# Kernel tuning notes

Hardware: AMD Instinct MI355X
Metric: run time of the kernel (lower is better)

Reference implementation:

```python
import jax, jax.numpy as jnp
import numpy as np

H, IN, D, RD, A = 1024, 14, 100000, 10, 2

def setup_inputs() -> dict:
    key = jax.random.key(0)
    ks = jax.random.split(key, 12)
    f = lambda k, shp, s=1.0: jax.random.normal(k, shp, dtype=jnp.float32) * s
    return {
        "x_t": f(ks[0], (1, IN)),
        "h": f(ks[1], (1, 1, H), 0.1),
        "c": f(ks[2], (1, 1, H), 0.1),
        "keys": f(ks[3], (D, RD)),
        "vals": f(ks[4], (D, H)),
        "W_i2h": f(ks[5], (5 * H, IN), 0.1),
        "b_i2h": jnp.zeros((5 * H,), jnp.float32),
        "W_h2h": f(ks[6], (5 * H, H), 0.03),
        "b_h2h": jnp.zeros((5 * H,), jnp.float32),
        "W_ih": f(ks[7], (H, H), 0.03),
        "b_ih": jnp.zeros((H,), jnp.float32),
        "W_actor": f(ks[8], (A, H), 0.03),
        "b_actor": jnp.zeros((A,), jnp.float32),
        "W_critic": f(ks[9], (1, H), 0.03),
        "b_critic": jnp.zeros((1,), jnp.float32),
        "pick_arm": 0,
    }


def reference(x_t, h, c, keys, vals, W_i2h, b_i2h, W_h2h, b_h2h,
              W_ih, b_ih, W_actor, b_actor, W_critic, b_critic, pick_arm):
    Hd = W_h2h.shape[1]
    Rd = keys.shape[1]
    h2 = h.reshape(h.shape[1], -1)   # [1, H]
    c2 = c.reshape(c.shape[1], -1)   # [1, H]
    # fused i2h + h2h preactivation: [1, 5H]
    preact = x_t @ W_i2h.T + b_i2h + h2 @ W_h2h.T + b_h2h
    gates = jax.nn.sigmoid(preact[:, :4 * Hd])
    f_t = gates[:, :Hd]
    i_t = gates[:, Hd:2 * Hd]
    o_t = gates[:, 2 * Hd:3 * Hd]
    r_t = gates[:, 3 * Hd:4 * Hd]
    c_new = jnp.tanh(preact[:, 4 * Hd:])
    c_t = f_t * c2 + i_t * c_new
    # DND read: cosine similarity over stored keys, softmax-weighted value sum
    q = jax.lax.dynamic_slice(x_t[0], (pick_arm * Rd,), (Rd,))  # retrieval key
    dots = keys @ q                                              # [D]
    denom = jnp.maximum(jnp.linalg.norm(keys, axis=1) * jnp.linalg.norm(q), 1e-8)
    w = jax.nn.softmax(dots / denom)                             # [D]
    m_t = jnp.tanh(w @ vals)                                     # [H]
    c_t = c_t + r_t * m_t
    h_t = o_t * jnp.tanh(c_t)
    # A2C head (standard dnd-lstm A2C): shared relu layer, actor softmax, critic scalar
    hh = jax.nn.relu(h_t @ W_ih.T + b_ih)
    pi = jax.nn.softmax(hh @ W_actor.T + b_actor, axis=-1)       # [1, A]
    v = hh @ W_critic.T + b_critic                               # [1, 1]
    # categorical sampling with a fixed key (replaces torch.distributions sample)
    a = jax.random.categorical(jax.random.key(1), jnp.log(pi[0]))
    logp = jnp.log(pi[0, a])
    # pack: [pi(A), v(1), log_prob(1), h_t(H), c_t(H)]
    return jnp.concatenate([pi[0], v[0], logp[None], h_t[0], c_t[0]])
```

## Files before the change

kernel.cpp:

```cpp
#include <hip/hip_runtime.h>
#include <math.h>

#define NHID 1024
#define NIN 14
#define NKEYS 100000
#define NRD 10
#define R3 100
#define NB3 1000
#define NBPRE 1280
#define NSLOT 16
#define NPF 10

typedef float f32x4 __attribute__((ext_vector_type(4)));
typedef float f32x2 __attribute__((ext_vector_type(2)));

#define WS_MACC    0
#define WS_L       16384
#define WS_PREACT  16400
#define WS_HH      21520
#define ZERO_BYTES ((16384 + NSLOT) * 4)

__device__ inline float wave_reduce_sum(float v) {
#pragma unroll
    for (int off = 32; off > 0; off >>= 1) v += __shfl_down(v, off, 64);
    return v;
}

__device__ inline float sigm(float x) { return 1.0f / (1.0f + expf(-x)); }

__device__ inline float bcast_lane(float v, int lane) {
    return __uint_as_float(__builtin_amdgcn_readlane(__float_as_uint(v), lane));
}

__device__ inline void atomAddF(float* p, float v) { unsafeAtomicAdd(p, v); }

__device__ inline float load_q(const float* __restrict__ x, int pick, float* q) {
    int start = pick * NRD;
    if (start > NIN - NRD) start = NIN - NRD;
    if (start < 0) start = 0;
    float qn = 0.f;
#pragma unroll
    for (int k = 0; k < NRD; ++k) { q[k] = x[start + k]; qn = fmaf(q[k], q[k], qn); }
    return sqrtf(qn);
}

__device__ inline float score2(const float* __restrict__ keys, int i,
                               const float* q, float qn) {
    const f32x2* kp = (const f32x2*)(keys + (size_t)i * NRD);
    float dot = 0.f, kn = 0.f;
#pragma unroll
    for (int k = 0; k < 5; ++k) {
        f32x2 kv = kp[k];
        dot = fmaf(kv.x, q[2 * k], fmaf(kv.y, q[2 * k + 1], dot));
        kn  = fmaf(kv.x, kv.x, fmaf(kv.y, kv.y, kn));
    }
    return dot / fmaxf(sqrtf(kn) * qn, 1e-8f);
}

__global__ void __launch_bounds__(256) kA(const float* __restrict__ keys,
                                          const float* __restrict__ x,
                                          const int* __restrict__ pick_arm,
                                          const float* __restrict__ vals,
                                          float* __restrict__ macc,
                                          float* __restrict__ Lacc,
                                          const float* __restrict__ h,
                                          const float* __restrict__ Wi,
                                          const float* __restrict__ bi,
                                          const float* __restrict__ Wh,
                                          const float* __restrict__ bh,
                                          float* __restrict__ preact) {
    int tid = threadIdx.x;
    if (blockIdx.x < NB3) {
        int r0 = blockIdx.x * R3;
        int slot = blockIdx.x & (NSLOT - 1);
        int lane = tid & 63;
        const f32x4* vp = (const f32x4*)vals + ((size_t)r0 << 8) + tid;
        f32x4 buf[NPF];
#pragma unroll
        for (int j = 0; j < NPF; ++j)
            buf[j] = __builtin_nontemporal_load(&vp[(size_t)j << 8]);
        float q[NRD];
        float qn = load_q(x, pick_arm[0], q);
        float wva = expf(score2(keys, r0 + lane, q, qn));
        float wvb = 0.f;
        if (lane < R3 - 64)
            wvb = expf(score2(keys, r0 + 64 + lane, q, qn));
        if (tid < 64) {
            float ls = wave_reduce_sum(wva + wvb);
            if (tid == 0) atomAddF(&Lacc[slot], ls);
        }
        float ax = 0.f, ay = 0.f, az = 0.f, aw = 0.f;
#pragma unroll
        for (int r = 0; r < R3; ++r) {
            float w = (r < 64) ? bcast_lane(wva, r) : bcast_lane(wvb, r - 64);
            f32x4 v = buf[r % NPF];
            if (r + NPF < R3)
                buf[r % NPF] = __builtin_nontemporal_load(&vp[(size_t)(r + NPF) << 8]);
            ax = fmaf(w, v.x, ax);
            ay = fmaf(w, v.y, ay);
            az = fmaf(w, v.z, az);
            aw = fmaf(w, v.w, aw);
        }
        float* ms = macc + (size_t)slot * NHID;
        atomAddF(&ms[4 * tid + 0], ax);
        atomAddF(&ms[4 * tid + 1], ay);
        atomAddF(&ms[4 * tid + 2], az);
        atomAddF(&ms[4 * tid + 3], aw);
    } else {
        int wave = tid >> 6, lane = tid & 63;
        int row = (blockIdx.x - NB3) * 4 + wave;
        const f32x4* w4 = (const f32x4*)(Wh + (size_t)row * NHID);
        const f32x4* h4 = (const f32x4*)h;
        float p = 0.f;
#pragma unroll
        for (int j = 0; j < 4; ++j) {
            f32x4 wv = __builtin_nontemporal_load(&w4[j * 64 + lane]);
            f32x4 hv = h4[j * 64 + lane];
            p += wv.x * hv.x + wv.y * hv.y + wv.z * hv.z + wv.w * hv.w;
        }
        if (lane < NIN) p += x[lane] * Wi[(size_t)row * NIN + lane];
        p = wave_reduce_sum(p);
        if (lane == 0) preact[row] = p + bi[row] + bh[row];
    }
}

__global__ void __launch_bounds__(256) k45(const float* __restrict__ preact,
                                           const float* __restrict__ macc,
                                           const float* __restrict__ Lacc,
                                           const float* __restrict__ c_in,
                                           const float* __restrict__ Wih,
                                           const float* __restrict__ bih,
                                           float* __restrict__ out,
                                           float* __restrict__ hh) {
    __shared__ float hlds[NHID];
    int tid = threadIdx.x;
    float Ls = 0.f;
#pragma unroll
    for (int s = 0; s < NSLOT; ++s) Ls += Lacc[s];
    float invL = 1.0f / Ls;
    const f32x4* pre4 = (const f32x4*)preact;
    f32x4 fg = pre4[tid];
    f32x4 ig = pre4[256 + tid];
    f32x4 og = pre4[512 + tid];
    f32x4 rg = pre4[768 + tid];
    f32x4 gg = pre4[1024 + tid];
    f32x4 m4 = {0.f, 0.f, 0.f, 0.f};
#pragma unroll
    for (int s = 0; s < NSLOT; ++s) m4 += ((const f32x4*)(macc + (size_t)s * NHID))[tid];
    f32x4 c4 = ((const f32x4*)c_in)[tid];
    f32x4 h4, ct4;
#pragma unroll
    for (int e = 0; e < 4; ++e) {
        float f = sigm(fg[e]);
        float i = sigm(ig[e]);
        float o = sigm(og[e]);
        float r = sigm(rg[e]);
        float cn = tanhf(gg[e]);
        float mt = tanhf(m4[e] * invL);
        float ct = f * c4[e] + i * cn + r * mt;
        ct4[e] = ct;
        h4[e] = o * tanhf(ct);
    }
    ((f32x4*)hlds)[tid] = h4;
    if (blockIdx.x == 0) {
        ((f32x4*)(out + 4))[tid] = h4;
        ((f32x4*)(out + 4 + NHID))[tid] = ct4;
    }
    __syncthreads();
    int wave = tid >> 6, lane = tid & 63;
    int row = blockIdx.x * 4 + wave;
    const f32x4* w4 = (const f32x4*)(Wih + (size_t)row * NHID);
    const f32x4* hl4 = (const f32x4*)hlds;
    float p = 0.f;
#pragma unroll
    for (int j = 0; j < 4; ++j) {
        f32x4 wv = __builtin_nontemporal_load(&w4[j * 64 + lane]);
        f32x4 hv = hl4[j * 64 + lane];
        p += wv.x * hv.x + wv.y * hv.y + wv.z * hv.z + wv.w * hv.w;
    }
    p = wave_reduce_sum(p);
    if (lane == 0) hh[row] = fmaxf(p + bih[row], 0.f);
}

#define TF_ROUND(r) { x0 += x1; x1 = (x1 << r) | (x1 >> (32 - r)); x1 ^= x0; }

__global__ void k6_heads(const float* __restrict__ hh, const float* __restrict__ Wa,
                         const float* __restrict__ ba, const float* __restrict__ Wc,
                         const float* __restrict__ bc, float* __restrict__ out) {
    __shared__ float zz[3];
    int wave = threadIdx.x >> 6, lane = threadIdx.x & 63;
    if (wave < 3) {
        const float* W = (wave == 2) ? Wc : Wa + wave * NHID;
        const f32x4* w4 = (const f32x4*)W;
        const f32x4* h4 = (const f32x4*)hh;
        float p = 0.f;
#pragma unroll
        for (int j = 0; j < 4; ++j) {
            f32x4 wv = w4[j * 64 + lane];
            f32x4 hv = h4[j * 64 + lane];
            p += wv.x * hv.x + wv.y * hv.y + wv.z * hv.z + wv.w * hv.w;
        }
        p = wave_reduce_sum(p);
        if (lane == 0) zz[wave] = p;
    }
    __syncthreads();
    if (threadIdx.x == 0) {
        float z0 = zz[0] + ba[0], z1 = zz[1] + ba[1], v = zz[2] + bc[0];
        float mz = fmaxf(z0, z1);
        float e0 = expf(z0 - mz), e1 = expf(z1 - mz);
        float sum = e0 + e1;
        float pi0 = e0 / sum, pi1 = e1 / sum;
        float lse = mz + logf(sum);
        unsigned ks0 = 0u, ks1 = 1u, ks2 = 0u ^ 1u ^ 0x1BD11BDAu;
        unsigned x0 = 0u + ks0, x1 = 1u + ks1;
        TF_ROUND(13) TF_ROUND(15) TF_ROUND(26) TF_ROUND(6)
        x0 += ks1; x1 += ks2 + 1u;
        TF_ROUND(17) TF_ROUND(29) TF_ROUND(16) TF_ROUND(24)
        x0 += ks2; x1 += ks0 + 2u;
        TF_ROUND(13) TF_ROUND(15) TF_ROUND(26) TF_ROUND(6)
        x0 += ks0; x1 += ks1 + 3u;
        TF_ROUND(17) TF_ROUND(29) TF_ROUND(16) TF_ROUND(24)
        x0 += ks1; x1 += ks2 + 4u;
        TF_ROUND(13) TF_ROUND(15) TF_ROUND(26) TF_ROUND(6)
        x0 += ks2; x1 += ks0 + 5u;
        float u0 = __uint_as_float((x0 >> 9) | 0x3F800000u) - 1.0f;
        float u1 = __uint_as_float((x1 >> 9) | 0x3F800000u) - 1.0f;
        const float tiny = 1.17549435e-38f;
        u0 = fmaxf(u0, tiny); u1 = fmaxf(u1, tiny);
        float g0 = -logf(-logf(u0));
        float g1 = -logf(-logf(u1));
        int a = (z1 + g1 > z0 + g0) ? 1 : 0;
        float logp = (a ? z1 : z0) - lse;
        out[0] = pi0; out[1] = pi1; out[2] = v; out[3] = logp;
    }
}

extern "C" void kernel_launch(void* const* d_in, const int* in_sizes, int n_in,
                              void* d_out, int out_size, void* d_ws, size_t ws_size,
                              hipStream_t stream) {
    const float* x      = (const float*)d_in[0];
    const float* h      = (const float*)d_in[1];
    const float* c      = (const float*)d_in[2];
    const float* keys   = (const float*)d_in[3];
    const float* vals   = (const float*)d_in[4];
    const float* Wi2h   = (const float*)d_in[5];
    const float* bi2h   = (const float*)d_in[6];
    const float* Wh2h   = (const float*)d_in[7];
    const float* bh2h   = (const float*)d_in[8];
    const float* Wih    = (const float*)d_in[9];
    const float* bih    = (const float*)d_in[10];
    const float* Wact   = (const float*)d_in[11];
    const float* bact   = (const float*)d_in[12];
    const float* Wcrit  = (const float*)d_in[13];
    const float* bcrit  = (const float*)d_in[14];
    const int*   pick   = (const int*)d_in[15];
    float* out = (float*)d_out;
    float* ws  = (float*)d_ws;

    (void)hipMemsetAsync(ws, 0, ZERO_BYTES, stream);
    kA<<<NB3 + NBPRE, 256, 0, stream>>>(keys, x, pick, vals,
                                        ws + WS_MACC, ws + WS_L,
                                        h, Wi2h, bi2h, Wh2h, bh2h, ws + WS_PREACT);
    k45<<<NHID / 4, 256, 0, stream>>>(ws + WS_PREACT, ws + WS_MACC, ws + WS_L,
                                      c, Wih, bih, out, ws + WS_HH);
    k6_heads<<<1, 256, 0, stream>>>(ws + WS_HH, Wact, bact, Wcrit, bcrit, out);
}
```

Baseline: 92.12 us.

## Double-bank grouped prefetch of vals rows and halve atomic accumulation slots

Replaces the rolling per-row prefetch ring with two register banks of ten rows each. The next group is loaded while the current group is consumed, and sched_barrier fences the phases so the compiler cannot reorder or collapse them. The number of partial-sum slots for the weighted value accumulation also drops from 16 to 8, which shrinks the zeroed workspace and the later reduction but raises atomic contention per slot. Keeping two banks live doubles the prefetch registers and may reduce occupancy.

```diff
diff --git a/kernel.cpp b/kernel.cpp
--- a/kernel.cpp
+++ b/kernel.cpp
@@ -8,17 +8,17 @@
 #define R3 100
 #define NB3 1000
 #define NBPRE 1280
-#define NSLOT 16
-#define NPF 10
+#define NSLOT 8
+#define GRP 10
 
 typedef float f32x4 __attribute__((ext_vector_type(4)));
 typedef float f32x2 __attribute__((ext_vector_type(2)));
 
 #define WS_MACC    0
-#define WS_L       16384
-#define WS_PREACT  16400
-#define WS_HH      21520
-#define ZERO_BYTES ((16384 + NSLOT) * 4)
+#define WS_L       8192
+#define WS_PREACT  8208
+#define WS_HH      13328
+#define ZERO_BYTES ((NSLOT * NHID + NSLOT) * 4)
 
 __device__ inline float wave_reduce_sum(float v) {
 #pragma unroll
@@ -75,10 +75,11 @@
         int slot = blockIdx.x & (NSLOT - 1);
         int lane = tid & 63;
         const f32x4* vp = (const f32x4*)vals + ((size_t)r0 << 8) + tid;
-        f32x4 buf[NPF];
-#pragma unroll
-        for (int j = 0; j < NPF; ++j)
-            buf[j] = __builtin_nontemporal_load(&vp[(size_t)j << 8]);
+        f32x4 bankA[GRP], bankB[GRP];
+#pragma unroll
+        for (int j = 0; j < GRP; ++j)
+            bankA[j] = __builtin_nontemporal_load(&vp[(size_t)j << 8]);
+        __builtin_amdgcn_sched_barrier(0);
         float q[NRD];
         float qn = load_q(x, pick_arm[0], q);
         float wva = expf(score2(keys, r0 + lane, q, qn));
@@ -91,15 +92,32 @@
         }
         float ax = 0.f, ay = 0.f, az = 0.f, aw = 0.f;
 #pragma unroll
-        for (int r = 0; r < R3; ++r) {
-            float w = (r < 64) ? bcast_lane(wva, r) : bcast_lane(wvb, r - 64);
-            f32x4 v = buf[r % NPF];
-            if (r + NPF < R3)
-                buf[r % NPF] = __builtin_nontemporal_load(&vp[(size_t)(r + NPF) << 8]);
-            ax = fmaf(w, v.x, ax);
-            ay = fmaf(w, v.y, ay);
-            az = fmaf(w, v.z, az);
-            aw = fmaf(w, v.w, aw);
+        for (int g = 0; g < R3 / GRP; ++g) {
+            if (g + 1 < R3 / GRP) {
+                if (g & 1) {
+#pragma unroll
+                    for (int j = 0; j < GRP; ++j)
+                        bankA[j] = __builtin_nontemporal_load(
+                            &vp[(size_t)((g + 1) * GRP + j) << 8]);
+                } else {
+#pragma unroll
+                    for (int j = 0; j < GRP; ++j)
+                        bankB[j] = __builtin_nontemporal_load(
+                            &vp[(size_t)((g + 1) * GRP + j) << 8]);
+                }
+            }
+            __builtin_amdgcn_sched_barrier(0);
+#pragma unroll
+            for (int j = 0; j < GRP; ++j) {
+                int r = g * GRP + j;
+                float w = (r < 64) ? bcast_lane(wva, r) : bcast_lane(wvb, r - 64);
+                f32x4 v = (g & 1) ? bankB[j] : bankA[j];
+                ax = fmaf(w, v.x, ax);
+                ay = fmaf(w, v.y, ay);
+                az = fmaf(w, v.z, az);
+                aw = fmaf(w, v.w, aw);
+            }
+            __builtin_amdgcn_sched_barrier(0);
         }
         float* ms = macc + (size_t)slot * NHID;
         atomAddF(&ms[4 * tid + 0], ax);
```

Result: faster. 90.28 us (median of 2 runs) (-2.0%).
